# Kernel optimization log

Hardware: AMD Instinct MI355X
Metric: run time of the kernel (lower is better)

Reference implementation:

```python
import jax, jax.numpy as jnp
import numpy as np

B, K, G = 1048576, 32, 8
SIGMA = 1.0


def setup_inputs() -> dict:
    key = jax.random.key(0)
    k1, k2 = jax.random.split(key)
    mu = jax.random.normal(k1, (B, K), dtype=jnp.float32)
    private_attribute = jax.random.randint(k2, (B,), 0, G, dtype=jnp.int64 if jax.config.jax_enable_x64 else jnp.int32)
    return {"mu": mu, "private_attribute": private_attribute}


def _gmm_loss(mu, labels):
    # --- segment reduce: per-label counts, means, covariances ---
    onehot = jax.nn.one_hot(labels, G, dtype=mu.dtype)          # [B,G]
    counts = jnp.sum(onehot, axis=0)                             # [G]
    mu_g = (onehot.T @ mu) / counts[:, None]                     # [G,K] group means
    diff = mu - mu_g[labels]                                     # [B,K] centered rows
    # Sigma_sum[g] = sum_{i in g} diff_i^T diff_i  (outer products)
    sigma_sum = jnp.einsum('bg,bi,bj->gij', onehot, diff, diff)  # [G,K,K]
    eye = jnp.eye(K, dtype=mu.dtype)
    sigma_g = SIGMA * eye + sigma_sum / counts[:, None, None]    # [G,K,K]

    # --- per-group inverse / logdet for Gaussian KL ---
    inv = jnp.linalg.inv(sigma_g)                                # [G,K,K]
    _, logdet = jnp.linalg.slogdet(sigma_g)                      # [G]

    # --- pairwise KL( N(u_i,S_i) || N(u_j,S_j) ) ---
    # tr(S_j^{-1} S_i)
    tr = jnp.einsum('jab,iba->ij', inv, sigma_g)                 # [G,G]
    d = mu_g[None, :, :] - mu_g[:, None, :]                      # d[i,j] = u_j - u_i
    mahal = jnp.einsum('ijd,jde,ije->ij', d, inv, d)             # [G,G]
    kl = 0.5 * (tr + mahal - K + logdet[None, :] - logdet[:, None])

    # original loop: for i in range(G-1): for j in range(1, G): if j != i
    idx = jnp.arange(G)
    mask = (idx[:, None] < G - 1) & (idx[None, :] >= 1) & (idx[:, None] != idx[None, :])
    w = counts[:, None] * counts[None, :]
    result = jnp.sum(jnp.where(mask, kl * w, jnp.zeros_like(kl)))
    return result / (float(B) ** 2)


def reference(mu, private_attribute):
    return _gmm_loss(mu, private_attribute)
```

## Files before the change

kernel.cpp:

```cpp
#include <hip/hip_runtime.h>
#include <math.h>

#define K 32
#define G 8
#define SIGMA_V 1.0f
#define RF __builtin_amdgcn_readfirstlane
#define RPB 512
#define RPW 128

#define RAW_OFF   0
#define MUSUM_OFF 8192
#define CNT_OFF   8448
#define ICNT_OFF  8456
#define CUR_OFF   8464
#define DONE_OFF  8472
#define DESC_OFF  8480
#define IDX_OFF   16384
#define HDR_INTS  16384

#define WAITV(n) asm volatile("s_waitcnt vmcnt(" #n ")" ::: "memory")
typedef __attribute__((address_space(3))) void lds_void;
typedef __attribute__((address_space(1))) void glb_void;
#define GLL(gsrc, ldst) __builtin_amdgcn_global_load_lds((const glb_void*)(gsrc), (lds_void*)(ldst), 16, 0, 0)

__global__ __launch_bounds__(256, 8) void gmm_hist(const int* __restrict__ lab,
                                                   float* __restrict__ ws,
                                                   int* __restrict__ wsI, int B, int nblk) {
  __shared__ int h[G];
  __shared__ int amLast;
  __shared__ int off[G], bb[G + 1], scnt[G];
  const int tid = threadIdx.x;
  if (tid < G) h[tid] = 0;
  __syncthreads();
  int c[G];
  #pragma unroll
  for (int g = 0; g < G; ++g) c[g] = 0;
  const int nt = gridDim.x * blockDim.x;
  const int4* lab4 = reinterpret_cast<const int4*>(lab);
  for (int i = blockIdx.x * blockDim.x + tid; i < B / 4; i += nt) {
    const int4 v = lab4[i];
    #pragma unroll
    for (int g = 0; g < G; ++g)
      c[g] += (v.x == g) + (v.y == g) + (v.z == g) + (v.w == g);
  }
  const int lane = tid & 63;
  #pragma unroll
  for (int g = 0; g < G; ++g) {
    int t = c[g];
    #pragma unroll
    for (int o = 32; o >= 1; o >>= 1) t += __shfl_xor(t, o);
    if (lane == 0) atomicAdd(&h[g], t);
  }
  __syncthreads();
  if (tid < G) atomicAdd(&wsI[ICNT_OFF + tid], h[tid]);
  __syncthreads();
  if (tid == 0) {
    __threadfence();
    amLast = (atomicAdd(&wsI[DONE_OFF], 1) == (int)gridDim.x - 1);
  }
  __syncthreads();
  if (!amLast) return;

  if (tid == 0) {
    int o = 0, b = 0;
    for (int g = 0; g < G; ++g) {
      const int cc = atomicAdd(&wsI[ICNT_OFF + g], 0);
      scnt[g] = cc; off[g] = o; bb[g] = b;
      ws[CNT_OFF + g] = (float)cc;
      wsI[CUR_OFF + g] = o;
      o = (o + cc + 15) & ~15;
      b += (cc + RPB - 1) / RPB;
    }
    bb[G] = b;
  }
  __syncthreads();
  for (int t = tid; t < nblk; t += blockDim.x) {
    int st = 0, cn = 0, gg = 0;
    #pragma unroll
    for (int g = 0; g < G; ++g) {
      if (t >= bb[g] && t < bb[g + 1]) {
        const int k = t - bb[g];
        st = off[g] + k * RPB;
        const int rem = scnt[g] - k * RPB;
        cn = rem < RPB ? rem : RPB;
        gg = g;
      }
    }
    wsI[DESC_OFF + 3 * t]     = st;
    wsI[DESC_OFF + 3 * t + 1] = cn;
    wsI[DESC_OFF + 3 * t + 2] = gg;
  }
}

__global__ __launch_bounds__(256, 8) void gmm_scatter(const int* __restrict__ lab,
                                                      int* __restrict__ wsI, int B) {
  __shared__ int lcnt[G], lofs[G + 1], lbase[G], lpos[G];
  __shared__ int sorted[1024];
  const int tid = threadIdx.x;
  const int base = blockIdx.x * 1024;
  if (tid < G) { lcnt[tid] = 0; lpos[tid] = 0; }
  __syncthreads();
  const int4 v = *reinterpret_cast<const int4*>(lab + base + tid * 4);
  atomicAdd(&lcnt[v.x], 1); atomicAdd(&lcnt[v.y], 1);
  atomicAdd(&lcnt[v.z], 1); atomicAdd(&lcnt[v.w], 1);
  __syncthreads();
  if (tid == 0) {
    int o = 0;
    #pragma unroll
    for (int g = 0; g < G; ++g) { lofs[g] = o; o += lcnt[g]; }
    lofs[G] = o;
  }
  __syncthreads();
  if (tid < G) lbase[tid] = atomicAdd(&wsI[CUR_OFF + tid], lcnt[tid]);
  int p;
  p = atomicAdd(&lpos[v.x], 1); sorted[lofs[v.x] + p] = base + tid * 4;
  p = atomicAdd(&lpos[v.y], 1); sorted[lofs[v.y] + p] = base + tid * 4 + 1;
  p = atomicAdd(&lpos[v.z], 1); sorted[lofs[v.z] + p] = base + tid * 4 + 2;
  p = atomicAdd(&lpos[v.w], 1); sorted[lofs[v.w] + p] = base + tid * 4 + 3;
  __syncthreads();
  for (int e = tid; e < 1024; e += 256) {
    const int val = sorted[e];
    int gg = 0;
    #pragma unroll
    for (int g = 1; g < G; ++g) gg += (e >= lofs[g]);
    wsI[IDX_OFF + lbase[gg] + (e - lofs[gg])] = val;
  }
}

#define OUTER(a, b) { \
  acc[0]=fmaf(a.x,b.x,acc[0]);   acc[1]=fmaf(a.x,b.y,acc[1]);   acc[2]=fmaf(a.x,b.z,acc[2]);   acc[3]=fmaf(a.x,b.w,acc[3]); \
  acc[4]=fmaf(a.y,b.x,acc[4]);   acc[5]=fmaf(a.y,b.y,acc[5]);   acc[6]=fmaf(a.y,b.z,acc[6]);   acc[7]=fmaf(a.y,b.w,acc[7]); \
  acc[8]=fmaf(a.z,b.x,acc[8]);   acc[9]=fmaf(a.z,b.y,acc[9]);   acc[10]=fmaf(a.z,b.z,acc[10]); acc[11]=fmaf(a.z,b.w,acc[11]); \
  acc[12]=fmaf(a.w,b.x,acc[12]); acc[13]=fmaf(a.w,b.y,acc[13]); acc[14]=fmaf(a.w,b.z,acc[14]); acc[15]=fmaf(a.w,b.w,acc[15]); \
  ms[0]+=b.x; ms[1]+=b.y; ms[2]+=b.z; ms[3]+=b.w; }

#define STAGE8(iv, bi) do { \
  float* db = &lds[wave * 1024 + (bi) * 256]; \
  GLL(mu + (size_t)(unsigned)(iv) * K + lf * 4, db); \
} while (0)

#define COMPUTE8(bi) do { \
  const float* sb = &lds[wave * 1024 + (bi) * 256]; \
  _Pragma("unroll") \
  for (int r = 0; r < 8; ++r) { \
    const float4 a  = *reinterpret_cast<const float4*>(&sb[r * 32 + i8 * 4]); \
    const float4 bv = *reinterpret_cast<const float4*>(&sb[r * 32 + j8 * 4]); \
    OUTER(a, bv); \
  } \
} while (0)

__global__ __launch_bounds__(256, 4) void gmm_stats3(const float* __restrict__ mu,
                                                     const int* __restrict__ wsI,
                                                     float* __restrict__ ws) {
  __shared__ float lds[4224];
  const int bd  = blockIdx.x * 3;
  const int s   = RF(wsI[DESC_OFF + bd]);
  const int cnt = RF(wsI[DESC_OFF + bd + 1]);
  const int g   = RF(wsI[DESC_OFF + bd + 2]);
  if (cnt <= 0) return;

  const int tid = threadIdx.x, wave = tid >> 6, lane = tid & 63;
  const int i8 = lane >> 3, j8 = lane & 7;
  const int lg8 = lane >> 3, lf = lane & 7;
  float acc[16], ms[4];
  #pragma unroll
  for (int e = 0; e < 16; ++e) acc[e] = 0.f;
  ms[0] = ms[1] = ms[2] = ms[3] = 0.f;

  int wcnt = cnt - wave * RPW;
  wcnt = wcnt < 0 ? 0 : (wcnt > RPW ? RPW : wcnt);
  const int* idxp = wsI + IDX_OFF + s + wave * RPW;
  const int nch = wcnt >> 3;

  if (nch == 16) {
    const int i0 = idxp[lg8];
    int inext    = idxp[8 + lg8];
    WAITV(1); STAGE8(i0, 0);
    {
      const int i1 = inext;
      inext = idxp[16 + lg8];
      WAITV(2); STAGE8(i1, 1);
    }
    {
      const int i2 = inext;
      inext = idxp[24 + lg8];
      WAITV(2); STAGE8(i2, 2);
    }
    #pragma unroll 1
    for (int k = 0; k < 12; ++k) {
      const int istage = inext;
      inext = idxp[(k + 4) * 8 + lg8];
      WAITV(2);
      STAGE8(istage, (k + 3) & 3);
      COMPUTE8(k & 3);
    }
    WAITV(1); STAGE8(inext, 15 & 3);
    COMPUTE8(12 & 3);
    COMPUTE8(13 & 3);
    WAITV(1); COMPUTE8(14 & 3);
    WAITV(0); COMPUTE8(15 & 3);
  } else {
    for (int k = 0; k < nch; ++k) {
      const int iv = idxp[k * 8 + lg8];
      WAITV(0); STAGE8(iv, k & 3);
      WAITV(0); COMPUTE8(k & 3);
    }
  }
  for (int q = nch << 3; q < wcnt; ++q) {
    const int r = idxp[q];
    const float* rp = mu + (size_t)(unsigned)r * K;
    const float4 a  = *reinterpret_cast<const float4*>(rp + i8 * 4);
    const float4 bv = *reinterpret_cast<const float4*>(rp + j8 * 4);
    OUTER(a, bv);
  }

  __syncthreads();
  #pragma unroll
  for (int e = 0; e < 16; ++e) lds[wave * 1056 + e * 64 + lane] = acc[e];
  if (i8 == 0) {
    #pragma unroll
    for (int e = 0; e < 4; ++e) lds[wave * 1056 + 1024 + j8 * 4 + e] = ms[e];
  }
  __syncthreads();
  for (int t = tid; t < 1056; t += 256) {
    const float sm = lds[t] + lds[1056 + t] + lds[2112 + t] + lds[3168 + t];
    if (t < 1024) {
      const int e = t >> 6, ln = t & 63;
      const int row = 4 * (ln >> 3) + (e >> 2), col = 4 * (ln & 7) + (e & 3);
      atomicAdd(ws + RAW_OFF + g * K * K + row * K + col, sm);
    } else {
      atomicAdd(ws + MUSUM_OFF + g * K + (t - 1024), sm);
    }
  }
}

#define ACC_CASE(gc_, Av, Bv_) do{ \
  facc[gc_][0]=fmaf(Av.x,Bv_.x,facc[gc_][0]); facc[gc_][1]=fmaf(Av.x,Bv_.y,facc[gc_][1]); \
  facc[gc_][2]=fmaf(Av.y,Bv_.x,facc[gc_][2]); facc[gc_][3]=fmaf(Av.y,Bv_.y,facc[gc_][3]); \
  if (a_blk==0){ msum[gc_][0]+=Bv_.x; msum[gc_][1]+=Bv_.y; } }while(0)
#define PROC(gv, Av, Bv_) switch(gv){ \
  case 0: ACC_CASE(0,Av,Bv_); break; case 1: ACC_CASE(1,Av,Bv_); break; \
  case 2: ACC_CASE(2,Av,Bv_); break; case 3: ACC_CASE(3,Av,Bv_); break; \
  case 4: ACC_CASE(4,Av,Bv_); break; case 5: ACC_CASE(5,Av,Bv_); break; \
  case 6: ACC_CASE(6,Av,Bv_); break; default: ACC_CASE(7,Av,Bv_); break; }

__global__ __launch_bounds__(256, 4) void gmm_stats_fb(const float* __restrict__ mu,
                                                       const int* __restrict__ lab,
                                                       float* __restrict__ ws, int B) {
  const int tid = threadIdx.x;
  const int a_blk = tid >> 4, b_blk = tid & 15;
  const int rpb = B / 1024;
  const long rbase = (long)blockIdx.x * rpb;
  float facc[G][4]; float msum[G][2];
  #pragma unroll
  for (int g = 0; g < G; ++g) { facc[g][0]=facc[g][1]=facc[g][2]=facc[g][3]=0.f; msum[g][0]=msum[g][1]=0.f; }
  const float2* __restrict__ mu2 = reinterpret_cast<const float2*>(mu);
  for (int q = 0; q < rpb; ++q) {
    const long r = rbase + q;
    const float2 Av = mu2[r * 16 + a_blk];
    const float2 Bv_ = mu2[r * 16 + b_blk];
    const int g0 = RF(lab[r]);
    PROC(g0, Av, Bv_);
  }
  const int arow = a_blk * 2, bcol = b_blk * 2;
  #pragma unroll
  for (int g = 0; g < G; ++g) {
    float* base = &ws[RAW_OFF + g * K * K];
    atomicAdd(base + (arow)*K + bcol, facc[g][0]);
    atomicAdd(base + (arow)*K + bcol + 1, facc[g][1]);
    atomicAdd(base + (arow+1)*K + bcol, facc[g][2]);
    atomicAdd(base + (arow+1)*K + bcol + 1, facc[g][3]);
  }
  if (a_blk == 0)
    #pragma unroll
    for (int g = 0; g < G; ++g) {
      atomicAdd(&ws[MUSUM_OFF + g*K + bcol], msum[g][0]);
      atomicAdd(&ws[MUSUM_OFF + g*K + bcol + 1], msum[g][1]);
    }
}

__global__ __launch_bounds__(512, 1) void gmm_finalize(const float* __restrict__ ws,
                                                       float* __restrict__ out, int B) {
  __shared__ double sig[G][K][K];
  __shared__ double inv[G][K][K];
  __shared__ double mg[G][K];
  __shared__ double ldet[G];
  __shared__ double cshared[G];
  __shared__ double pairsum[G];
  const int tid = threadIdx.x;
  const int w = tid >> 6;
  const int lane = tid & 63;

  if (tid < G) cshared[tid] = (double)ws[CNT_OFF + tid];
  __syncthreads();
  const double cinv = 1.0 / cshared[w];
  if (lane < K) mg[w][lane] = (double)ws[MUSUM_OFF + w * K + lane] * cinv;
  __syncthreads();
  for (int e = lane; e < K * K; e += 64) {
    const int a = e >> 5, b = e & 31;
    double s = (double)ws[RAW_OFF + w * K * K + e] * cinv - mg[w][a] * mg[w][b];
    if (a == b) s += (double)SIGMA_V;
    sig[w][a][b] = s;
  }
  __syncthreads();

  const int c = lane & 31;
  double col[K];
  #pragma unroll
  for (int i2 = 0; i2 < K; ++i2) {
    double sv = sig[w][i2][c];
    col[i2] = (lane < K) ? sv : ((i2 == c) ? 1.0 : 0.0);
  }
  double ld = 0.0;
  #pragma unroll
  for (int j2 = 0; j2 < K; ++j2) {
    double rowj = col[j2];
    double p = __shfl(rowj, j2);
    double pinv = 1.0 / p;
    ld += log(p);
    double scaled = rowj * pinv;
    #pragma unroll
    for (int i2 = 0; i2 < K; ++i2) {
      if (i2 == j2) continue;
      double bij = __shfl(col[i2], j2);
      col[i2] = fma(-bij, scaled, col[i2]);
    }
    col[j2] = scaled;
  }
  if (lane >= K) {
    #pragma unroll
    for (int i2 = 0; i2 < K; ++i2) inv[w][i2][lane - K] = col[i2];
  }
  if (lane == 0) ldet[w] = ld;
  __syncthreads();

  double accp = 0.0;
  for (int jj = 0; jj < G; ++jj) {
    const bool ok = (w < G - 1) && (jj >= 1) && (w != jj);
    if (ok) {
      double t = 0.0;
      for (int e = lane; e < K * K; e += 64) {
        const int a = e >> 5, b = e & 31;
        const double da = mg[jj][a] - mg[w][a];
        const double db = mg[jj][b] - mg[w][b];
        t += inv[jj][a][b] * (sig[w][a][b] + da * db);
      }
      #pragma unroll
      for (int off = 32; off >= 1; off >>= 1) t += __shfl_xor(t, off);
      if (lane == 0) accp += 0.5 * (t - (double)K + ldet[jj] - ldet[w]) * cshared[w] * cshared[jj];
    }
  }
  if (lane == 0) pairsum[w] = accp;
  __syncthreads();
  if (tid == 0) {
    double tot = 0.0;
    #pragma unroll
    for (int q = 0; q < G; ++q) tot += pairsum[q];
    const double Bf = (double)B;
    out[0] = (float)(tot / (Bf * Bf));
  }
}

extern "C" void kernel_launch(void* const* d_in, const int* in_sizes, int n_in,
                              void* d_out, int out_size, void* d_ws, size_t ws_size,
                              hipStream_t stream) {
  const float* mu = (const float*)d_in[0];
  const int* lab = (const int*)d_in[1];
  float* ws = (float*)d_ws;
  int* wsI = (int*)d_ws;
  float* out = (float*)d_out;
  const int B = in_sizes[1];

  hipMemsetAsync(d_ws, 0, (size_t)DESC_OFF * 4, stream);

  const size_t need = (size_t)(HDR_INTS + B + 16 * G + 32) * 4;
  if (ws_size >= need) {
    const int nblk = (B + RPB - 1) / RPB + G;
    hipLaunchKernelGGL(gmm_hist, dim3(256), dim3(256), 0, stream, lab, ws, wsI, B, nblk);
    hipLaunchKernelGGL(gmm_scatter, dim3(B / 1024), dim3(256), 0, stream, lab, wsI, B);
    hipLaunchKernelGGL(gmm_stats3, dim3(nblk), dim3(256), 0, stream, mu, wsI, ws);
  } else {
    hipLaunchKernelGGL(gmm_hist, dim3(256), dim3(256), 0, stream, lab, ws, wsI, B, 0);
    hipLaunchKernelGGL(gmm_stats_fb, dim3(1024), dim3(256), 0, stream, mu, lab, ws, B);
  }
  hipLaunchKernelGGL(gmm_finalize, dim3(1), dim3(512), 0, stream, ws, out, B);
}
```

Measured before the change: 219.0 us.

## Issue all row gathers up front into large LDS buffer with asm ds_read batches

The stats kernel now stages each wave's full 128-row chunk into a 64KB LDS buffer by issuing all 16 global-to-LDS loads up front, instead of running a 4-slot rolling pipeline. It then consumes the data in pairs using graded vmcnt waits and batched inline-asm ds_read_b128 reads with explicit lgkmcnt waits. The aim is more memory-level parallelism for the random row gathers and less LDS read latency per outer-product step. The larger LDS footprint lowers occupancy to 2 blocks per CU. The fallback paths get bounds fixes for B not divisible by 1024, and the partial-chunk path contains a leftover no-op asm read.

```diff
diff --git a/kernel.cpp b/kernel.cpp
--- a/kernel.cpp
+++ b/kernel.cpp
@@ -20,8 +20,13 @@
 
 #define WAITV(n) asm volatile("s_waitcnt vmcnt(" #n ")" ::: "memory")
 typedef __attribute__((address_space(3))) void lds_void;
+typedef __attribute__((address_space(3))) float lds_float;
 typedef __attribute__((address_space(1))) void glb_void;
 #define GLL(gsrc, ldst) __builtin_amdgcn_global_load_lds((const glb_void*)(gsrc), (lds_void*)(ldst), 16, 0, 0)
+
+typedef float f32x4 __attribute__((ext_vector_type(4)));
+#define DSR(d, base, OFF) \
+  asm volatile("ds_read_b128 %0, %1 offset:%2" : "=v"(d) : "v"(base), "i"(OFF))
 
 __global__ __launch_bounds__(256, 8) void gmm_hist(const int* __restrict__ lab,
                                                    float* __restrict__ ws,
@@ -134,25 +139,27 @@
   acc[12]=fmaf(a.w,b.x,acc[12]); acc[13]=fmaf(a.w,b.y,acc[13]); acc[14]=fmaf(a.w,b.z,acc[14]); acc[15]=fmaf(a.w,b.w,acc[15]); \
   ms[0]+=b.x; ms[1]+=b.y; ms[2]+=b.z; ms[3]+=b.w; }
 
-#define STAGE8(iv, bi) do { \
-  float* db = &lds[wave * 1024 + (bi) * 256]; \
-  GLL(mu + (size_t)(unsigned)(iv) * K + lf * 4, db); \
+#define ROWS4(OFF) do { \
+  f32x4 a0,b0,a1,b1,a2,b2,a3,b3; \
+  DSR(a0, abase, OFF);       DSR(b0, bbase, OFF); \
+  DSR(a1, abase, (OFF)+128); DSR(b1, bbase, (OFF)+128); \
+  DSR(a2, abase, (OFF)+256); DSR(b2, bbase, (OFF)+256); \
+  DSR(a3, abase, (OFF)+384); DSR(b3, bbase, (OFF)+384); \
+  asm volatile("s_waitcnt lgkmcnt(0)" ::: "memory"); \
+  __builtin_amdgcn_sched_barrier(0); \
+  OUTER(a0, b0); OUTER(a1, b1); OUTER(a2, b2); OUTER(a3, b3); \
 } while (0)
 
-#define COMPUTE8(bi) do { \
-  const float* sb = &lds[wave * 1024 + (bi) * 256]; \
-  _Pragma("unroll") \
-  for (int r = 0; r < 8; ++r) { \
-    const float4 a  = *reinterpret_cast<const float4*>(&sb[r * 32 + i8 * 4]); \
-    const float4 bv = *reinterpret_cast<const float4*>(&sb[r * 32 + j8 * 4]); \
-    OUTER(a, bv); \
-  } \
+#define CPAIR(WN, OFF) do { \
+  WAITV(WN); \
+  ROWS4(OFF); ROWS4((OFF)+512); ROWS4((OFF)+1024); ROWS4((OFF)+1536); \
 } while (0)
 
-__global__ __launch_bounds__(256, 4) void gmm_stats3(const float* __restrict__ mu,
+__global__ __launch_bounds__(256, 2) void gmm_stats5(const float* __restrict__ mu,
                                                      const int* __restrict__ wsI,
                                                      float* __restrict__ ws) {
-  __shared__ float lds[4224];
+  __shared__ float stg[16384];
+  __shared__ int idxl[512];
   const int bd  = blockIdx.x * 3;
   const int s   = RF(wsI[DESC_OFF + bd]);
   const int cnt = RF(wsI[DESC_OFF + bd + 1]);
@@ -170,60 +177,63 @@
   int wcnt = cnt - wave * RPW;
   wcnt = wcnt < 0 ? 0 : (wcnt > RPW ? RPW : wcnt);
   const int* idxp = wsI + IDX_OFF + s + wave * RPW;
-  const int nch = wcnt >> 3;
-
-  if (nch == 16) {
-    const int i0 = idxp[lg8];
-    int inext    = idxp[8 + lg8];
-    WAITV(1); STAGE8(i0, 0);
-    {
-      const int i1 = inext;
-      inext = idxp[16 + lg8];
-      WAITV(2); STAGE8(i1, 1);
-    }
-    {
-      const int i2 = inext;
-      inext = idxp[24 + lg8];
-      WAITV(2); STAGE8(i2, 2);
-    }
-    #pragma unroll 1
-    for (int k = 0; k < 12; ++k) {
-      const int istage = inext;
-      inext = idxp[(k + 4) * 8 + lg8];
-      WAITV(2);
-      STAGE8(istage, (k + 3) & 3);
-      COMPUTE8(k & 3);
-    }
-    WAITV(1); STAGE8(inext, 15 & 3);
-    COMPUTE8(12 & 3);
-    COMPUTE8(13 & 3);
-    WAITV(1); COMPUTE8(14 & 3);
-    WAITV(0); COMPUTE8(15 & 3);
+  float* wstg = &stg[wave * 4096];
+  const unsigned wbase = (unsigned)(size_t)(lds_float*)wstg;
+  const unsigned abase = wbase + i8 * 16;
+  const unsigned bbase = wbase + j8 * 16;
+
+  if (wcnt == RPW) {
+    const int ia = idxp[lane];
+    const int ib = idxp[64 + lane];
+    WAITV(0);
+    idxl[wave * 128 + lane] = ia;
+    idxl[wave * 128 + 64 + lane] = ib;
+    #pragma unroll
+    for (int c = 0; c < 16; ++c) {
+      const int m = idxl[wave * 128 + c * 8 + lg8];
+      GLL(mu + (size_t)(unsigned)m * K + lf * 4, wstg + c * 256);
+    }
+    CPAIR(14, 0);      CPAIR(12, 2048);  CPAIR(10, 4096);  CPAIR(8, 6144);
+    CPAIR(6, 8192);    CPAIR(4, 10240);  CPAIR(2, 12288);  CPAIR(0, 14336);
   } else {
+    const int nch = wcnt >> 3;
     for (int k = 0; k < nch; ++k) {
       const int iv = idxp[k * 8 + lg8];
-      WAITV(0); STAGE8(iv, k & 3);
-      WAITV(0); COMPUTE8(k & 3);
-    }
-  }
-  for (int q = nch << 3; q < wcnt; ++q) {
-    const int r = idxp[q];
-    const float* rp = mu + (size_t)(unsigned)r * K;
-    const float4 a  = *reinterpret_cast<const float4*>(rp + i8 * 4);
-    const float4 bv = *reinterpret_cast<const float4*>(rp + j8 * 4);
-    OUTER(a, bv);
-  }
-
-  __syncthreads();
-  #pragma unroll
-  for (int e = 0; e < 16; ++e) lds[wave * 1056 + e * 64 + lane] = acc[e];
+      WAITV(0);
+      GLL(mu + (size_t)(unsigned)iv * K + lf * 4, wstg);
+      WAITV(0);
+      f32x4 a0, b0;
+      #pragma unroll
+      for (int r = 0; r < 8; ++r) {
+        DSR(a0, abase, 0); DSR(b0, bbase, 0);
+        (void)a0; (void)b0;
+        break;
+      }
+      for (int r = 0; r < 8; ++r) {
+        const float4 a = *reinterpret_cast<const float4*>(&wstg[r * 32 + i8 * 4]);
+        const float4 bv = *reinterpret_cast<const float4*>(&wstg[r * 32 + j8 * 4]);
+        OUTER(a, bv);
+      }
+    }
+    for (int q = nch << 3; q < wcnt; ++q) {
+      const int r = idxp[q];
+      const float* rp = mu + (size_t)(unsigned)r * K;
+      const float4 a  = *reinterpret_cast<const float4*>(rp + i8 * 4);
+      const float4 bv = *reinterpret_cast<const float4*>(rp + j8 * 4);
+      OUTER(a, bv);
+    }
+  }
+
+  __syncthreads();
+  #pragma unroll
+  for (int e = 0; e < 16; ++e) stg[wave * 1056 + e * 64 + lane] = acc[e];
   if (i8 == 0) {
     #pragma unroll
-    for (int e = 0; e < 4; ++e) lds[wave * 1056 + 1024 + j8 * 4 + e] = ms[e];
+    for (int e = 0; e < 4; ++e) stg[wave * 1056 + 1024 + j8 * 4 + e] = ms[e];
   }
   __syncthreads();
   for (int t = tid; t < 1056; t += 256) {
-    const float sm = lds[t] + lds[1056 + t] + lds[2112 + t] + lds[3168 + t];
+    const float sm = stg[t] + stg[1056 + t] + stg[2112 + t] + stg[3168 + t];
     if (t < 1024) {
       const int e = t >> 6, ln = t & 63;
       const int row = 4 * (ln >> 3) + (e >> 2), col = 4 * (ln & 7) + (e & 3);
@@ -249,14 +259,13 @@
                                                        float* __restrict__ ws, int B) {
   const int tid = threadIdx.x;
   const int a_blk = tid >> 4, b_blk = tid & 15;
-  const int rpb = B / 1024;
+  const int rpb = (B + 1023) / 1024;
   const long rbase = (long)blockIdx.x * rpb;
   float facc[G][4]; float msum[G][2];
   #pragma unroll
   for (int g = 0; g < G; ++g) { facc[g][0]=facc[g][1]=facc[g][2]=facc[g][3]=0.f; msum[g][0]=msum[g][1]=0.f; }
   const float2* __restrict__ mu2 = reinterpret_cast<const float2*>(mu);
-  for (int q = 0; q < rpb; ++q) {
-    const long r = rbase + q;
+  for (long r = rbase; r < rbase + rpb && r < B; ++r) {
     const float2 Av = mu2[r * 16 + a_blk];
     const float2 Bv_ = mu2[r * 16 + b_blk];
     const int g0 = RF(lab[r]);
@@ -374,11 +383,11 @@
   hipMemsetAsync(d_ws, 0, (size_t)DESC_OFF * 4, stream);
 
   const size_t need = (size_t)(HDR_INTS + B + 16 * G + 32) * 4;
-  if (ws_size >= need) {
+  if (ws_size >= need && (B & 1023) == 0) {
     const int nblk = (B + RPB - 1) / RPB + G;
     hipLaunchKernelGGL(gmm_hist, dim3(256), dim3(256), 0, stream, lab, ws, wsI, B, nblk);
     hipLaunchKernelGGL(gmm_scatter, dim3(B / 1024), dim3(256), 0, stream, lab, wsI, B);
-    hipLaunchKernelGGL(gmm_stats3, dim3(nblk), dim3(256), 0, stream, mu, wsI, ws);
+    hipLaunchKernelGGL(gmm_stats5, dim3(nblk), dim3(256), 0, stream, mu, wsI, ws);
   } else {
     hipLaunchKernelGGL(gmm_hist, dim3(256), dim3(256), 0, stream, lab, ws, wsI, B, 0);
     hipLaunchKernelGGL(gmm_stats_fb, dim3(1024), dim3(256), 0, stream, mu, lab, ws, B);
```

New measurement: 238.6 us. 8.9% more time.

## Split last-block prep into separate kernel and scatter indices directly without LDS sort

Applied to the files above, without the earlier changes.

Replaces the last-block-done atomic pattern in the histogram kernel with a separate single-block prep kernel that computes group offsets and block descriptors. The scatter kernel no longer builds a locally sorted index buffer in LDS and writes each index straight to its global group slot. It also adds bounds guards for B not divisible by 1024 in the fallback path. The aim is to remove the threadfence/atomic completion check and an LDS staging pass, at the cost of one extra kernel launch and less coalesced global writes in scatter.

```diff
diff --git a/kernel.cpp b/kernel.cpp
--- a/kernel.cpp
+++ b/kernel.cpp
@@ -13,7 +13,6 @@
 #define CNT_OFF   8448
 #define ICNT_OFF  8456
 #define CUR_OFF   8464
-#define DONE_OFF  8472
 #define DESC_OFF  8480
 #define IDX_OFF   16384
 #define HDR_INTS  16384
@@ -24,52 +23,45 @@
 #define GLL(gsrc, ldst) __builtin_amdgcn_global_load_lds((const glb_void*)(gsrc), (lds_void*)(ldst), 16, 0, 0)
 
 __global__ __launch_bounds__(256, 8) void gmm_hist(const int* __restrict__ lab,
-                                                   float* __restrict__ ws,
-                                                   int* __restrict__ wsI, int B, int nblk) {
+                                                   int* __restrict__ wsI, int B) {
   __shared__ int h[G];
-  __shared__ int amLast;
-  __shared__ int off[G], bb[G + 1], scnt[G];
-  const int tid = threadIdx.x;
-  if (tid < G) h[tid] = 0;
+  if (threadIdx.x < G) h[threadIdx.x] = 0;
   __syncthreads();
   int c[G];
   #pragma unroll
   for (int g = 0; g < G; ++g) c[g] = 0;
   const int nt = gridDim.x * blockDim.x;
   const int4* lab4 = reinterpret_cast<const int4*>(lab);
-  for (int i = blockIdx.x * blockDim.x + tid; i < B / 4; i += nt) {
+  for (int i = blockIdx.x * blockDim.x + threadIdx.x; i < B / 4; i += nt) {
     const int4 v = lab4[i];
     #pragma unroll
     for (int g = 0; g < G; ++g)
       c[g] += (v.x == g) + (v.y == g) + (v.z == g) + (v.w == g);
   }
-  const int lane = tid & 63;
+  const int lane = threadIdx.x & 63;
   #pragma unroll
   for (int g = 0; g < G; ++g) {
     int t = c[g];
     #pragma unroll
-    for (int o = 32; o >= 1; o >>= 1) t += __shfl_xor(t, o);
+    for (int off = 32; off >= 1; off >>= 1) t += __shfl_xor(t, off);
     if (lane == 0) atomicAdd(&h[g], t);
   }
   __syncthreads();
-  if (tid < G) atomicAdd(&wsI[ICNT_OFF + tid], h[tid]);
-  __syncthreads();
-  if (tid == 0) {
-    __threadfence();
-    amLast = (atomicAdd(&wsI[DONE_OFF], 1) == (int)gridDim.x - 1);
-  }
-  __syncthreads();
-  if (!amLast) return;
-
+  if (threadIdx.x < G) atomicAdd(&wsI[ICNT_OFF + threadIdx.x], h[threadIdx.x]);
+}
+
+__global__ void gmm_prep(float* __restrict__ ws, int* __restrict__ wsI, int B, int nblk) {
+  __shared__ int off[G], bb[G + 1], scnt[G];
+  const int tid = threadIdx.x;
   if (tid == 0) {
     int o = 0, b = 0;
     for (int g = 0; g < G; ++g) {
-      const int cc = atomicAdd(&wsI[ICNT_OFF + g], 0);
-      scnt[g] = cc; off[g] = o; bb[g] = b;
-      ws[CNT_OFF + g] = (float)cc;
+      const int c = wsI[ICNT_OFF + g];
+      scnt[g] = c; off[g] = o; bb[g] = b;
+      ws[CNT_OFF + g] = (float)c;
       wsI[CUR_OFF + g] = o;
-      o = (o + cc + 15) & ~15;
-      b += (cc + RPB - 1) / RPB;
+      o = (o + c + 15) & ~15;
+      b += (c + RPB - 1) / RPB;
     }
     bb[G] = b;
   }
@@ -94,8 +86,7 @@
 
 __global__ __launch_bounds__(256, 8) void gmm_scatter(const int* __restrict__ lab,
                                                       int* __restrict__ wsI, int B) {
-  __shared__ int lcnt[G], lofs[G + 1], lbase[G], lpos[G];
-  __shared__ int sorted[1024];
+  __shared__ int lcnt[G], lbase[G], lpos[G];
   const int tid = threadIdx.x;
   const int base = blockIdx.x * 1024;
   if (tid < G) { lcnt[tid] = 0; lpos[tid] = 0; }
@@ -104,27 +95,13 @@
   atomicAdd(&lcnt[v.x], 1); atomicAdd(&lcnt[v.y], 1);
   atomicAdd(&lcnt[v.z], 1); atomicAdd(&lcnt[v.w], 1);
   __syncthreads();
-  if (tid == 0) {
-    int o = 0;
-    #pragma unroll
-    for (int g = 0; g < G; ++g) { lofs[g] = o; o += lcnt[g]; }
-    lofs[G] = o;
-  }
-  __syncthreads();
   if (tid < G) lbase[tid] = atomicAdd(&wsI[CUR_OFF + tid], lcnt[tid]);
+  __syncthreads();
   int p;
-  p = atomicAdd(&lpos[v.x], 1); sorted[lofs[v.x] + p] = base + tid * 4;
-  p = atomicAdd(&lpos[v.y], 1); sorted[lofs[v.y] + p] = base + tid * 4 + 1;
-  p = atomicAdd(&lpos[v.z], 1); sorted[lofs[v.z] + p] = base + tid * 4 + 2;
-  p = atomicAdd(&lpos[v.w], 1); sorted[lofs[v.w] + p] = base + tid * 4 + 3;
-  __syncthreads();
-  for (int e = tid; e < 1024; e += 256) {
-    const int val = sorted[e];
-    int gg = 0;
-    #pragma unroll
-    for (int g = 1; g < G; ++g) gg += (e >= lofs[g]);
-    wsI[IDX_OFF + lbase[gg] + (e - lofs[gg])] = val;
-  }
+  p = atomicAdd(&lpos[v.x], 1); wsI[IDX_OFF + lbase[v.x] + p] = base + tid * 4;
+  p = atomicAdd(&lpos[v.y], 1); wsI[IDX_OFF + lbase[v.y] + p] = base + tid * 4 + 1;
+  p = atomicAdd(&lpos[v.z], 1); wsI[IDX_OFF + lbase[v.z] + p] = base + tid * 4 + 2;
+  p = atomicAdd(&lpos[v.w], 1); wsI[IDX_OFF + lbase[v.w] + p] = base + tid * 4 + 3;
 }
 
 #define OUTER(a, b) { \
@@ -249,14 +226,13 @@
                                                        float* __restrict__ ws, int B) {
   const int tid = threadIdx.x;
   const int a_blk = tid >> 4, b_blk = tid & 15;
-  const int rpb = B / 1024;
+  const int rpb = (B + 1023) / 1024;
   const long rbase = (long)blockIdx.x * rpb;
   float facc[G][4]; float msum[G][2];
   #pragma unroll
   for (int g = 0; g < G; ++g) { facc[g][0]=facc[g][1]=facc[g][2]=facc[g][3]=0.f; msum[g][0]=msum[g][1]=0.f; }
   const float2* __restrict__ mu2 = reinterpret_cast<const float2*>(mu);
-  for (int q = 0; q < rpb; ++q) {
-    const long r = rbase + q;
+  for (long r = rbase; r < rbase + rpb && r < B; ++r) {
     const float2 Av = mu2[r * 16 + a_blk];
     const float2 Bv_ = mu2[r * 16 + b_blk];
     const int g0 = RF(lab[r]);
@@ -374,13 +350,15 @@
   hipMemsetAsync(d_ws, 0, (size_t)DESC_OFF * 4, stream);
 
   const size_t need = (size_t)(HDR_INTS + B + 16 * G + 32) * 4;
-  if (ws_size >= need) {
+  if (ws_size >= need && (B & 1023) == 0) {
     const int nblk = (B + RPB - 1) / RPB + G;
-    hipLaunchKernelGGL(gmm_hist, dim3(256), dim3(256), 0, stream, lab, ws, wsI, B, nblk);
+    hipLaunchKernelGGL(gmm_hist, dim3(256), dim3(256), 0, stream, lab, wsI, B);
+    hipLaunchKernelGGL(gmm_prep, dim3(1), dim3(256), 0, stream, ws, wsI, B, nblk);
     hipLaunchKernelGGL(gmm_scatter, dim3(B / 1024), dim3(256), 0, stream, lab, wsI, B);
     hipLaunchKernelGGL(gmm_stats3, dim3(nblk), dim3(256), 0, stream, mu, wsI, ws);
   } else {
-    hipLaunchKernelGGL(gmm_hist, dim3(256), dim3(256), 0, stream, lab, ws, wsI, B, 0);
+    hipLaunchKernelGGL(gmm_hist, dim3(256), dim3(256), 0, stream, lab, wsI, B);
+    hipLaunchKernelGGL(gmm_prep, dim3(1), dim3(256), 0, stream, ws, wsI, B, 0);
     hipLaunchKernelGGL(gmm_stats_fb, dim3(1024), dim3(256), 0, stream, mu, lab, ws, B);
   }
   hipLaunchKernelGGL(gmm_finalize, dim3(1), dim3(512), 0, stream, ws, out, B);
```

Result: no change. 215.3 us (-1.7%).
